# Performance work log

Hardware: AMD Instinct MI355X
Metric: run time of the kernel (lower is better)

The kernel has to match this reference:

```python
import jax, jax.numpy as jnp
import numpy as np

N, S, F, E, H, O, L, FE = 8, 1024, 64, 512, 8, 64, 6, 4
HD = E // H
FF = FE * E


def setup_inputs() -> dict:
    key = jax.random.key(0)
    ks = iter(jax.random.split(key, 40))
    def rn(shape, s=0.02):
        return jax.random.normal(next(ks), shape, jnp.float32) * s
    return {
        'x': jax.random.normal(next(ks), (N, F, S), jnp.float32),
        'W_first': rn((F, E)), 'b_first': jnp.zeros((E,), jnp.float32),
        'pos_emb': rn((S, E)),
        'Wq': rn((L, HD, HD)), 'bq': jnp.zeros((L, HD), jnp.float32),
        'Wk': rn((L, HD, HD)), 'bk': jnp.zeros((L, HD), jnp.float32),
        'Wv': rn((L, HD, HD)), 'bv': jnp.zeros((L, HD), jnp.float32),
        'Wo': rn((L, E, E)), 'bo': jnp.zeros((L, E), jnp.float32),
        'g1': jnp.ones((L, E), jnp.float32), 'be1': jnp.zeros((L, E), jnp.float32),
        'Wf1': rn((L, E, FF)), 'bf1': jnp.zeros((L, FF), jnp.float32),
        'Wf2': rn((L, FF, E)), 'bf2': jnp.zeros((L, E), jnp.float32),
        'g2': jnp.ones((L, E), jnp.float32), 'be2': jnp.zeros((L, E), jnp.float32),
        'Wfin': rn((E, O)), 'bfin': jnp.zeros((O,), jnp.float32),
    }


def layernorm(x, g, b, eps=1e-5):
    m = jnp.mean(x, axis=-1, keepdims=True)
    v = jnp.mean(jnp.square(x - m), axis=-1, keepdims=True)
    return (x - m) * jax.lax.rsqrt(v + eps) * g + b


def reference(x, W_first, b_first, pos_emb, Wq, bq, Wk, bk, Wv, bv, Wo, bo,
              g1, be1, Wf1, bf1, Wf2, bf2, g2, be2, Wfin, bfin):
    # x: (N, F, S) -> (N, S, F)
    h = jax.nn.relu(jnp.einsum('nfs,fe->nse', x, W_first) + b_first) + pos_emb[None]
    scale = E ** 0.5  # note: module scales by sqrt(embed_size), not sqrt(head_dim)
    for i in range(L):
        t = h.reshape(N, S, H, HD)
        q = jnp.einsum('nshd,de->nshe', t, Wq[i]) + bq[i]
        k = jnp.einsum('nshd,de->nshe', t, Wk[i]) + bk[i]
        v = jnp.einsum('nshd,de->nshe', t, Wv[i]) + bv[i]
        energy = jnp.einsum('nqhd,nkhd->nhqk', q, k)  # (N,H,S,S)
        att = jax.nn.softmax(energy / scale, axis=-1)
        o = jnp.einsum('nhqk,nkhd->nqhd', att, v).reshape(N, S, E)
        o = jnp.einsum('nse,ef->nsf', o, Wo[i]) + bo[i]
        hx = layernorm(o + h, g1[i], be1[i])
        ff = jax.nn.relu(jnp.einsum('nse,ef->nsf', hx, Wf1[i]) + bf1[i])
        ff = jnp.einsum('nsf,fe->nse', ff, Wf2[i]) + bf2[i]
        h = layernorm(ff + hx, g2[i], be2[i])
    # Conv1d kernel_size=1 == pointwise linear over channels; output (N, O, S)
    return jnp.einsum('nse,eo->nos', h, Wfin) + bfin[None, :, None]
```

## Files before the change

kernel.cpp:

```cpp
#include <hip/hip_runtime.h>
#include <hip/hip_bf16.h>
#include <math.h>

#define N_ 8
#define S_ 1024
#define F_ 64
#define E_ 512
#define H_ 8
#define O_ 64
#define L_ 6
#define HD_ 64
#define FF_ 2048
#define SCALE_ 0.044194173824159216f
#define LOG2E_ 1.4426950408889634f
#define QSCALE_ (SCALE_ * LOG2E_)

typedef unsigned short u16;
typedef __attribute__((ext_vector_type(8))) unsigned short u16x8;
typedef __attribute__((ext_vector_type(8))) short short8;
typedef __attribute__((ext_vector_type(4))) float floatx4;

__device__ __forceinline__ u16 f2b(float f) {
    union { float f; unsigned u; } v; v.f = f;
    unsigned u = v.u;
    unsigned r = (u + 0x7FFFu + ((u >> 16) & 1u)) >> 16;
    return (u16)r;
}
__device__ __forceinline__ u16 f2b_fast(float f) {
    union { float f; unsigned u; } v; v.f = f;
    return (u16)((v.u + 0x8000u) >> 16);
}
__device__ __forceinline__ int pperm(int row) {
    return ((2 * (row >> 2) + 5 * (row & 3)) & 7) | ((row & 2) << 2);
}

__global__ __launch_bounds__(256) void first_mfma(
    const float* __restrict__ x, const u16* __restrict__ wt,
    const float* __restrict__ bf, const float* __restrict__ pe,
    float* __restrict__ hout, u16* __restrict__ hb)
{
    __shared__ u16 a_s[128][72];
    int t = threadIdx.x;
    int w = t >> 6, lane = t & 63, quad = lane >> 4, c16 = lane & 15;
    int rowhalf = w >> 1, colhalf = w & 1;
    int col0 = blockIdx.x * 128;
    int row0 = blockIdx.y * 128;
    int n = row0 >> 10, s0 = row0 & 1023;

    const float* xb = x + (size_t)n * F_ * S_ + s0;
    #pragma unroll
    for (int i = 0; i < 8; i++) {
        int pos = (t + i * 256) * 4;
        int f = pos >> 7, sl = pos & 127;
        float4 v = *(const float4*)&xb[(size_t)f * S_ + sl];
        a_s[sl + 0][f] = f2b_fast(v.x);
        a_s[sl + 1][f] = f2b_fast(v.y);
        a_s[sl + 2][f] = f2b_fast(v.z);
        a_s[sl + 3][f] = f2b_fast(v.w);
    }
    __syncthreads();

    floatx4 acc[4][4];
    #pragma unroll
    for (int mt = 0; mt < 4; mt++)
        #pragma unroll
        for (int nt = 0; nt < 4; nt++) acc[mt][nt] = (floatx4){0.f, 0.f, 0.f, 0.f};

    #pragma unroll
    for (int ks = 0; ks < 2; ks++) {
        short8 af[4], bfr[4];
        #pragma unroll
        for (int mt = 0; mt < 4; mt++)
            af[mt] = *(const short8*)&a_s[rowhalf * 64 + mt * 16 + c16][ks * 32 + quad * 8];
        #pragma unroll
        for (int nt = 0; nt < 4; nt++)
            bfr[nt] = *(const short8*)&wt[(size_t)(col0 + colhalf * 64 + nt * 16 + c16) * F_
                                          + ks * 32 + quad * 8];
        #pragma unroll
        for (int mt = 0; mt < 4; mt++)
            #pragma unroll
            for (int nt = 0; nt < 4; nt++)
                acc[mt][nt] = __builtin_amdgcn_mfma_f32_16x16x32_bf16(
                    af[mt], bfr[nt], acc[mt][nt], 0, 0, 0);
    }

    #pragma unroll
    for (int nt = 0; nt < 4; nt++) {
        int col = col0 + colhalf * 64 + nt * 16 + c16;
        float bv = bf[col];
        #pragma unroll
        for (int mt = 0; mt < 4; mt++) {
            #pragma unroll
            for (int r = 0; r < 4; r++) {
                size_t row = (size_t)row0 + rowhalf * 64 + mt * 16 + quad * 4 + r;
                int s = (int)(row & 1023);
                float v = fmaxf(acc[mt][nt][r] + bv, 0.f) + pe[(size_t)s * E_ + col];
                hout[row * E_ + col] = v;
                hb[row * E_ + col] = f2b_fast(v);
            }
        }
    }
}

__global__ __launch_bounds__(256) void wcast_t(
    const float* __restrict__ W0, u16* __restrict__ Wt0, int K, int Nc)
{
    __shared__ float tile[32][33];
    int t = threadIdx.x;
    int bx = blockIdx.x, by = blockIdx.y;
    const float* W = W0 + (size_t)blockIdx.z * K * Nc;
    u16* Wt = Wt0 + (size_t)blockIdx.z * K * Nc;
    #pragma unroll
    for (int i = 0; i < 4; i++) {
        int q = t + i * 256; int r = q >> 5, c = q & 31;
        tile[r][c] = W[(size_t)(by * 32 + r) * Nc + bx * 32 + c];
    }
    __syncthreads();
    #pragma unroll
    for (int i = 0; i < 4; i++) {
        int q = t + i * 256; int r = q >> 5, c = q & 31;
        Wt[(size_t)(bx * 32 + r) * K + by * 32 + c] = f2b(tile[c][r]);
    }
}

__global__ __launch_bounds__(256) void qkvw_cast(
    const float* __restrict__ Wq, const float* __restrict__ Wk,
    const float* __restrict__ Wv,
    u16* __restrict__ wqt, u16* __restrict__ wkt, u16* __restrict__ wvt)
{
    int l = blockIdx.x;
    int t = threadIdx.x;
    size_t off = (size_t)l * HD_ * HD_;
    #pragma unroll
    for (int i = 0; i < 16; i++) {
        int idx = t + i * 256;
        int e = idx >> 6, d = idx & 63;
        wqt[off + idx] = f2b(Wq[off + d * HD_ + e]);
        wkt[off + idx] = f2b(Wk[off + d * HD_ + e]);
        wvt[off + idx] = f2b(Wv[off + d * HD_ + e]);
    }
}

__global__ __launch_bounds__(256) void qkv_mfma(
    const u16* __restrict__ hb,
    const u16* __restrict__ wqt, const u16* __restrict__ wkt,
    const u16* __restrict__ wvt,
    const float* __restrict__ bq, const float* __restrict__ bk,
    const float* __restrict__ bv,
    u16* __restrict__ qo, u16* __restrict__ ko, u16* __restrict__ vo)
{
    __shared__ u16 a_s[256][72];
    int t = threadIdx.x;
    int w = t >> 6, lane = t & 63, quad = lane >> 4, c16 = lane & 15;
    size_t row0 = (size_t)blockIdx.x * 256;

    #pragma unroll
    for (int i = 0; i < 8; i++) {
        int q = t + i * 256; int r = q >> 3, c = q & 7;
        *(u16x8*)&a_s[r][c * 8] = *(const u16x8*)&hb[(row0 + r) * HD_ + c * 8];
    }
    __syncthreads();

    short8 af[4][2];
    #pragma unroll
    for (int mt = 0; mt < 4; mt++)
        #pragma unroll
        for (int ks = 0; ks < 2; ks++)
            af[mt][ks] = *(const short8*)&a_s[w * 64 + mt * 16 + c16][ks * 32 + quad * 8];

    const u16* wts[3] = {wqt, wkt, wvt};
    const float* bs[3] = {bq, bk, bv};
    u16* outs[3] = {qo, ko, vo};

    #pragma unroll
    for (int m = 0; m < 3; m++) {
        short8 bfr[4][2];
        #pragma unroll
        for (int nt = 0; nt < 4; nt++)
            #pragma unroll
            for (int ks = 0; ks < 2; ks++)
                bfr[nt][ks] = *(const short8*)&wts[m][(nt * 16 + c16) * HD_ + ks * 32 + quad * 8];
        floatx4 acc[4][4];
        #pragma unroll
        for (int mt = 0; mt < 4; mt++)
            #pragma unroll
            for (int nt = 0; nt < 4; nt++) acc[mt][nt] = (floatx4){0.f, 0.f, 0.f, 0.f};
        #pragma unroll
        for (int ks = 0; ks < 2; ks++)
            #pragma unroll
            for (int mt = 0; mt < 4; mt++)
                #pragma unroll
                for (int nt = 0; nt < 4; nt++)
                    acc[mt][nt] = __builtin_amdgcn_mfma_f32_16x16x32_bf16(
                        af[mt][ks], bfr[nt][ks], acc[mt][nt], 0, 0, 0);
        float osc = (m == 0) ? QSCALE_ : 1.0f;
        #pragma unroll
        for (int nt = 0; nt < 4; nt++) {
            float bv_ = bs[m][nt * 16 + c16];
            #pragma unroll
            for (int mt = 0; mt < 4; mt++)
                #pragma unroll
                for (int r = 0; r < 4; r++)
                    outs[m][(row0 + w * 64 + mt * 16 + quad * 4 + r) * HD_ + nt * 16 + c16] =
                        f2b_fast((acc[mt][nt][r] + bv_) * osc);
        }
    }
}

__global__ __launch_bounds__(256) void vtrans(
    const u16* __restrict__ vb, u16* __restrict__ vt)
{
    int bid = blockIdx.x;
    int st = bid & 15, hh = (bid >> 4) & 7, n = bid >> 7;
    __shared__ u16 tile[64][72];
    int t = threadIdx.x;
    #pragma unroll
    for (int i = 0; i < 2; i++) {
        int q = t + i * 256; int sl = q >> 3, c = q & 7;
        *(u16x8*)&tile[sl][c * 8] =
            *(const u16x8*)&vb[(((size_t)(n * S_ + st * 64 + sl)) * H_ + hh) * 64 + c * 8];
    }
    __syncthreads();
    #pragma unroll
    for (int i = 0; i < 2; i++) {
        int q = t + i * 256; int d = q >> 3, sc = q & 7;
        u16x8 v;
        #pragma unroll
        for (int j = 0; j < 8; j++) v[j] = tile[sc * 8 + j][d];
        *(u16x8*)&vt[((size_t)(n * H_ + hh) * 64 + d) * (size_t)S_ + st * 64 + sc * 8] = v;
    }
}

__global__ __launch_bounds__(256, 2) void attn_mfma(
    const u16* __restrict__ Q, const u16* __restrict__ K,
    const u16* __restrict__ Vt, u16* __restrict__ O)
{
    int bid = blockIdx.x;
    int qt = bid & 7, hh = (bid >> 3) & 7, n = bid >> 6;
    int t = threadIdx.x;
    int w = t >> 6, lane = t & 63, quad = lane >> 4, c16 = lane & 15;

    __shared__ u16 q_s[128][72];
    __shared__ u16 k_s[64][72];
    __shared__ u16 vt_s[64][72];
    __shared__ u16 p_s[4][32][72];

    const size_t qkbase = (size_t)n * S_ * E_ + hh * 64;
    const size_t vtbase = ((size_t)(n * H_ + hh) * 64) * (size_t)S_;

    #pragma unroll
    for (int i = 0; i < 4; i++) {
        int q = t + i * 256; int r = q >> 3, c = q & 7;
        *(u16x8*)&q_s[r][c * 8] =
            *(const u16x8*)&Q[qkbase + (size_t)(qt * 128 + r) * E_ + c * 8];
    }
    __syncthreads();

    short8 af[2][2];
    #pragma unroll
    for (int mt = 0; mt < 2; mt++)
        #pragma unroll
        for (int ks = 0; ks < 2; ks++)
            af[mt][ks] = *(const short8*)&q_s[w * 32 + mt * 16 + c16][ks * 32 + quad * 8];

    const short8 ones = {(short)0x3F80, (short)0x3F80, (short)0x3F80, (short)0x3F80,
                         (short)0x3F80, (short)0x3F80, (short)0x3F80, (short)0x3F80};
    const int pr = pperm(c16);
    int pw[4];
    #pragma unroll
    for (int r = 0; r < 4; r++) pw[r] = pperm(quad * 4 + r);

    floatx4 oacc[2][4], lacc[2];
    #pragma unroll
    for (int mt = 0; mt < 2; mt++) {
        lacc[mt] = (floatx4){0.f, 0.f, 0.f, 0.f};
        #pragma unroll
        for (int nt = 0; nt < 4; nt++) oacc[mt][nt] = (floatx4){0.f, 0.f, 0.f, 0.f};
    }

    for (int k0 = 0; k0 < S_; k0 += 64) {
        #pragma unroll
        for (int i = 0; i < 2; i++) {
            int q = t + i * 256; int r = q >> 3, c = q & 7;
            *(u16x8*)&k_s[r][c * 8] =
                *(const u16x8*)&K[qkbase + (size_t)(k0 + r) * E_ + c * 8];
            *(u16x8*)&vt_s[r][c * 8] =
                *(const u16x8*)&Vt[vtbase + (size_t)r * S_ + k0 + c * 8];
        }
        __syncthreads();

        floatx4 sc[2][4];
        #pragma unroll
        for (int mt = 0; mt < 2; mt++)
            #pragma unroll
            for (int nt = 0; nt < 4; nt++) sc[mt][nt] = (floatx4){0.f, 0.f, 0.f, 0.f};
        #pragma unroll
        for (int ks = 0; ks < 2; ks++) {
            short8 bfr[4];
            #pragma unroll
            for (int nt = 0; nt < 4; nt++)
                bfr[nt] = *(const short8*)&k_s[nt * 16 + c16][ks * 32 + quad * 8];
            #pragma unroll
            for (int mt = 0; mt < 2; mt++)
                #pragma unroll
                for (int nt = 0; nt < 4; nt++)
                    sc[mt][nt] = __builtin_amdgcn_mfma_f32_16x16x32_bf16(
                        af[mt][ks], bfr[nt], sc[mt][nt], 0, 0, 0);
        }

        #pragma unroll
        for (int mt = 0; mt < 2; mt++)
            #pragma unroll
            for (int nt = 0; nt < 4; nt++)
                #pragma unroll
                for (int r = 0; r < 4; r++)
                    p_s[w][mt * 16 + pw[r]][nt * 16 + c16] =
                        f2b_fast(exp2f(sc[mt][nt][r]));

        #pragma unroll
        for (int ks = 0; ks < 2; ks++) {
            short8 vf[4];
            #pragma unroll
            for (int nt = 0; nt < 4; nt++)
                vf[nt] = *(const short8*)&vt_s[nt * 16 + c16][ks * 32 + quad * 8];
            #pragma unroll
            for (int mt = 0; mt < 2; mt++) {
                short8 pf = *(const short8*)&p_s[w][mt * 16 + pr][ks * 32 + quad * 8];
                lacc[mt] = __builtin_amdgcn_mfma_f32_16x16x32_bf16(pf, ones, lacc[mt], 0, 0, 0);
                #pragma unroll
                for (int nt = 0; nt < 4; nt++)
                    oacc[mt][nt] = __builtin_amdgcn_mfma_f32_16x16x32_bf16(
                        pf, vf[nt], oacc[mt][nt], 0, 0, 0);
            }
        }
        __syncthreads();
    }

    #pragma unroll
    for (int mt = 0; mt < 2; mt++)
        #pragma unroll
        for (int r = 0; r < 4; r++) {
            float rl = 1.f / lacc[mt][r];
            int s = qt * 128 + w * 32 + mt * 16 + quad * 4 + r;
            size_t base = (size_t)(n * S_ + s) * E_ + hh * 64;
            #pragma unroll
            for (int nt = 0; nt < 4; nt++)
                O[base + nt * 16 + c16] = f2b_fast(oacc[mt][nt][r] * rl);
        }
}

template <bool RELU, bool HASRES, bool OUTF32, bool OUTBF16>
__global__ __launch_bounds__(256) void gemm_mfma(
    const u16* __restrict__ A, const u16* __restrict__ Bt,
    const float* __restrict__ bias, const float* __restrict__ resid,
    float* __restrict__ outf, u16* __restrict__ outb, int M, int Nc, int K)
{
    __shared__ u16 a_s[128][72];
    __shared__ u16 b_s[128][72];
    int t = threadIdx.x;
    int w = t >> 6, lane = t & 63, quad = lane >> 4, c16 = lane & 15;
    int rowhalf = w >> 1, colhalf = w & 1;
    size_t row0 = (size_t)blockIdx.y * 128;
    size_t col0 = (size_t)blockIdx.x * 128;

    floatx4 acc[4][4];
    #pragma unroll
    for (int mt = 0; mt < 4; mt++)
        #pragma unroll
        for (int nt = 0; nt < 4; nt++) acc[mt][nt] = (floatx4){0.f, 0.f, 0.f, 0.f};

    for (int k0 = 0; k0 < K; k0 += 64) {
        #pragma unroll
        for (int i = 0; i < 4; i++) {
            int q = t + i * 256; int r = q >> 3, c = q & 7;
            *(u16x8*)&a_s[r][c * 8] = *(const u16x8*)&A[(row0 + r) * K + k0 + c * 8];
            *(u16x8*)&b_s[r][c * 8] = *(const u16x8*)&Bt[(col0 + r) * K + k0 + c * 8];
        }
        __syncthreads();
        #pragma unroll
        for (int ks = 0; ks < 2; ks++) {
            short8 af[4], bf[4];
            #pragma unroll
            for (int mt = 0; mt < 4; mt++)
                af[mt] = *(const short8*)&a_s[rowhalf * 64 + mt * 16 + c16][ks * 32 + quad * 8];
            #pragma unroll
            for (int nt = 0; nt < 4; nt++)
                bf[nt] = *(const short8*)&b_s[colhalf * 64 + nt * 16 + c16][ks * 32 + quad * 8];
            #pragma unroll
            for (int mt = 0; mt < 4; mt++)
                #pragma unroll
                for (int nt = 0; nt < 4; nt++)
                    acc[mt][nt] = __builtin_amdgcn_mfma_f32_16x16x32_bf16(
                        af[mt], bf[nt], acc[mt][nt], 0, 0, 0);
        }
        __syncthreads();
    }

    #pragma unroll
    for (int nt = 0; nt < 4; nt++) {
        int col = (int)col0 + colhalf * 64 + nt * 16 + c16;
        float bv = bias[col];
        #pragma unroll
        for (int mt = 0; mt < 4; mt++) {
            size_t rowb = row0 + rowhalf * 64 + mt * 16 + quad * 4;
            #pragma unroll
            for (int r = 0; r < 4; r++) {
                size_t row = rowb + r;
                float v = acc[mt][nt][r] + bv;
                if constexpr (HASRES) v += resid[row * Nc + col];
                if constexpr (RELU) v = fmaxf(v, 0.f);
                if constexpr (OUTF32) outf[row * Nc + col] = v;
                if constexpr (OUTBF16) outb[row * Nc + col] = f2b_fast(v);
            }
        }
    }
}

template <bool EMITB>
__global__ __launch_bounds__(256) void layernorm_k(
    const float* __restrict__ in, const float* __restrict__ g,
    const float* __restrict__ bb, float* __restrict__ out, u16* __restrict__ outb)
{
    int row = blockIdx.x;
    int t = threadIdx.x;
    const float* x = in + (size_t)row * E_;
    float x0 = x[t], x1 = x[t + 256];
    float s = x0 + x1;
    #pragma unroll
    for (int off = 32; off; off >>= 1) s += __shfl_down(s, off, 64);
    __shared__ float red[4];
    int wid = t >> 6, lane = t & 63;
    if (lane == 0) red[wid] = s;
    __syncthreads();
    float m = (red[0] + red[1] + red[2] + red[3]) * (1.f / E_);
    float d0 = x0 - m, d1 = x1 - m;
    float sq = d0 * d0 + d1 * d1;
    #pragma unroll
    for (int off = 32; off; off >>= 1) sq += __shfl_down(sq, off, 64);
    __syncthreads();
    if (lane == 0) red[wid] = sq;
    __syncthreads();
    float var = (red[0] + red[1] + red[2] + red[3]) * (1.f / E_);
    float rstd = rsqrtf(var + 1e-5f);
    float o0 = d0 * rstd * g[t] + bb[t];
    float o1 = d1 * rstd * g[t + 256] + bb[t + 256];
    out[(size_t)row * E_ + t] = o0;
    out[(size_t)row * E_ + t + 256] = o1;
    if constexpr (EMITB) {
        outb[(size_t)row * E_ + t] = f2b_fast(o0);
        outb[(size_t)row * E_ + t + 256] = f2b_fast(o1);
    }
}

__global__ __launch_bounds__(256) void final_mfma(
    const u16* __restrict__ hb, const u16* __restrict__ wft,
    const float* __restrict__ bfin, float* __restrict__ outp)
{
    __shared__ u16 a_s[64][72];
    int t = threadIdx.x;
    int w = t >> 6, lane = t & 63, quad = lane >> 4, c16 = lane & 15;
    size_t row0 = (size_t)blockIdx.x * 64;

    floatx4 acc[4];
    #pragma unroll
    for (int nt = 0; nt < 4; nt++) acc[nt] = (floatx4){0.f, 0.f, 0.f, 0.f};

    for (int k0 = 0; k0 < E_; k0 += 64) {
        #pragma unroll
        for (int i = 0; i < 2; i++) {
            int q = t + i * 256; int r = q >> 3, c = q & 7;
            *(u16x8*)&a_s[r][c * 8] = *(const u16x8*)&hb[(row0 + r) * E_ + k0 + c * 8];
        }
        __syncthreads();
        #pragma unroll
        for (int ks = 0; ks < 2; ks++) {
            short8 af = *(const short8*)&a_s[w * 16 + c16][ks * 32 + quad * 8];
            #pragma unroll
            for (int nt = 0; nt < 4; nt++) {
                short8 bf = *(const short8*)&wft[(nt * 16 + c16) * E_ + k0 + ks * 32 + quad * 8];
                acc[nt] = __builtin_amdgcn_mfma_f32_16x16x32_bf16(af, bf, acc[nt], 0, 0, 0);
            }
        }
        __syncthreads();
    }

    #pragma unroll
    for (int nt = 0; nt < 4; nt++) {
        int o = nt * 16 + c16;
        float bv = bfin[o];
        #pragma unroll
        for (int r = 0; r < 4; r++) {
            size_t row = row0 + w * 16 + quad * 4 + r;
            int n = (int)(row >> 10), s = (int)(row & 1023);
            outp[((size_t)(n * O_ + o)) * S_ + s] = acc[nt][r] + bv;
        }
    }
}

extern "C" void kernel_launch(void* const* d_in, const int* in_sizes, int n_in,
                              void* d_out, int out_size, void* d_ws, size_t ws_size,
                              hipStream_t stream)
{
    const float* x       = (const float*)d_in[0];
    const float* W_first = (const float*)d_in[1];
    const float* b_first = (const float*)d_in[2];
    const float* pos_emb = (const float*)d_in[3];
    const float* Wq      = (const float*)d_in[4];
    const float* bq      = (const float*)d_in[5];
    const float* Wk      = (const float*)d_in[6];
    const float* bk      = (const float*)d_in[7];
    const float* Wv      = (const float*)d_in[8];
    const float* bv      = (const float*)d_in[9];
    const float* Wo      = (const float*)d_in[10];
    const float* bo      = (const float*)d_in[11];
    const float* g1      = (const float*)d_in[12];
    const float* be1     = (const float*)d_in[13];
    const float* Wf1     = (const float*)d_in[14];
    const float* bf1     = (const float*)d_in[15];
    const float* Wf2     = (const float*)d_in[16];
    const float* bf2     = (const float*)d_in[17];
    const float* g2      = (const float*)d_in[18];
    const float* be2     = (const float*)d_in[19];
    const float* Wfin    = (const float*)d_in[20];
    const float* bfin    = (const float*)d_in[21];
    float* out = (float*)d_out;

    const size_t M4 = (size_t)N_ * S_ * E_;
    float* hbuf = (float*)d_ws;
    float* t1   = hbuf + M4;
    float* hx   = t1 + M4;
    u16*   hxb  = (u16*)(hx + M4);
    u16*   hb   = hxb;
    u16*   qb   = hxb + M4;
    u16*   kb   = qb + M4;
    u16*   vb   = kb + M4;
    u16*   vt   = vb + M4;
    u16*   ob   = vt + M4;
    u16*   ffb  = qb;
    u16*   wot  = ob + M4;
    u16*   wf1t = wot + (size_t)L_ * E_ * E_;
    u16*   wf2t = wf1t + (size_t)L_ * E_ * FF_;
    u16*   wqt  = wf2t + (size_t)L_ * FF_ * E_;
    u16*   wkt  = wqt + (size_t)L_ * HD_ * HD_;
    u16*   wvt  = wkt + (size_t)L_ * HD_ * HD_;
    u16*   wft  = wvt + (size_t)L_ * HD_ * HD_;
    u16*   w1t  = wft + (size_t)O_ * E_;

    const int rows = N_ * S_;

    qkvw_cast<<<L_, 256, 0, stream>>>(Wq, Wk, Wv, wqt, wkt, wvt);
    wcast_t<<<dim3(E_ / 32, F_ / 32, 1), 256, 0, stream>>>(W_first, w1t, F_, E_);
    wcast_t<<<dim3(E_ / 32, E_ / 32, L_), 256, 0, stream>>>(Wo, wot, E_, E_);
    wcast_t<<<dim3(FF_ / 32, E_ / 32, L_), 256, 0, stream>>>(Wf1, wf1t, E_, FF_);
    wcast_t<<<dim3(E_ / 32, FF_ / 32, L_), 256, 0, stream>>>(Wf2, wf2t, FF_, E_);
    wcast_t<<<dim3(O_ / 32, E_ / 32, 1), 256, 0, stream>>>(Wfin, wft, E_, O_);

    first_mfma<<<dim3(E_ / 128, rows / 128), 256, 0, stream>>>(
        x, w1t, b_first, pos_emb, hbuf, hb);

    for (int i = 0; i < L_; i++) {
        qkv_mfma<<<256, 256, 0, stream>>>(
            hb, wqt + (size_t)i * HD_ * HD_, wkt + (size_t)i * HD_ * HD_,
            wvt + (size_t)i * HD_ * HD_, bq + i * HD_, bk + i * HD_, bv + i * HD_,
            qb, kb, vb);
        vtrans<<<1024, 256, 0, stream>>>(vb, vt);
        attn_mfma<<<512, 256, 0, stream>>>(qb, kb, vt, ob);
        gemm_mfma<false, true, true, false><<<dim3(E_ / 128, rows / 128), 256, 0, stream>>>(
            ob, wot + (size_t)i * E_ * E_, bo + i * E_, hbuf, t1, nullptr, rows, E_, E_);
        layernorm_k<true><<<rows, 256, 0, stream>>>(t1, g1 + i * E_, be1 + i * E_, hx, hxb);
        gemm_mfma<true, false, false, true><<<dim3(FF_ / 128, rows / 128), 256, 0, stream>>>(
            hxb, wf1t + (size_t)i * E_ * FF_, bf1 + i * FF_, nullptr, nullptr, ffb,
            rows, FF_, E_);
        gemm_mfma<false, true, true, false><<<dim3(E_ / 128, rows / 128), 256, 0, stream>>>(
            ffb, wf2t + (size_t)i * FF_ * E_, bf2 + i * E_, hx, t1, nullptr,
            rows, E_, FF_);
        layernorm_k<true><<<rows, 256, 0, stream>>>(t1, g2 + i * E_, be2 + i * E_, hbuf, hb);
    }

    final_mfma<<<rows / 64, 256, 0, stream>>>(hb, wft, bfin, out);
}
```

Before: 1.157 ms.

## Register-prefetch next K tiles in GEMM/attention loops and halve M tile for E-wide GEMMs

```diff
diff --git a/kernel.cpp b/kernel.cpp
--- a/kernel.cpp
+++ b/kernel.cpp
@@ -278,14 +278,26 @@
         for (int nt = 0; nt < 4; nt++) oacc[mt][nt] = (floatx4){0.f, 0.f, 0.f, 0.f};
     }
 
+    int ar = t >> 3, acq = (t & 7) * 8;
+    u16x8 pk[2], pv[2];
+    #pragma unroll
+    for (int i = 0; i < 2; i++) {
+        pk[i] = *(const u16x8*)&K[qkbase + (size_t)(ar + i * 32) * E_ + acq];
+        pv[i] = *(const u16x8*)&Vt[vtbase + (size_t)(ar + i * 32) * S_ + acq];
+    }
+
     for (int k0 = 0; k0 < S_; k0 += 64) {
         #pragma unroll
         for (int i = 0; i < 2; i++) {
-            int q = t + i * 256; int r = q >> 3, c = q & 7;
-            *(u16x8*)&k_s[r][c * 8] =
-                *(const u16x8*)&K[qkbase + (size_t)(k0 + r) * E_ + c * 8];
-            *(u16x8*)&vt_s[r][c * 8] =
-                *(const u16x8*)&Vt[vtbase + (size_t)r * S_ + k0 + c * 8];
+            *(u16x8*)&k_s[ar + i * 32][acq] = pk[i];
+            *(u16x8*)&vt_s[ar + i * 32][acq] = pv[i];
+        }
+        if (k0 + 64 < S_) {
+            #pragma unroll
+            for (int i = 0; i < 2; i++) {
+                pk[i] = *(const u16x8*)&K[qkbase + (size_t)(k0 + 64 + ar + i * 32) * E_ + acq];
+                pv[i] = *(const u16x8*)&Vt[vtbase + (size_t)(ar + i * 32) * S_ + k0 + 64 + acq];
+            }
         }
         __syncthreads();
 
@@ -349,45 +361,63 @@
         }
 }
 
-template <bool RELU, bool HASRES, bool OUTF32, bool OUTBF16>
+template <int MT, bool RELU, bool HASRES, bool OUTF32, bool OUTBF16>
 __global__ __launch_bounds__(256) void gemm_mfma(
     const u16* __restrict__ A, const u16* __restrict__ Bt,
     const float* __restrict__ bias, const float* __restrict__ resid,
     float* __restrict__ outf, u16* __restrict__ outb, int M, int Nc, int K)
 {
-    __shared__ u16 a_s[128][72];
+    constexpr int MTILES = MT / 32;
+    __shared__ u16 a_s[MT][72];
     __shared__ u16 b_s[128][72];
     int t = threadIdx.x;
     int w = t >> 6, lane = t & 63, quad = lane >> 4, c16 = lane & 15;
     int rowhalf = w >> 1, colhalf = w & 1;
-    size_t row0 = (size_t)blockIdx.y * 128;
+    size_t row0 = (size_t)blockIdx.y * MT;
     size_t col0 = (size_t)blockIdx.x * 128;
 
-    floatx4 acc[4][4];
-    #pragma unroll
-    for (int mt = 0; mt < 4; mt++)
+    floatx4 acc[MTILES][4];
+    #pragma unroll
+    for (int mt = 0; mt < MTILES; mt++)
         #pragma unroll
         for (int nt = 0; nt < 4; nt++) acc[mt][nt] = (floatx4){0.f, 0.f, 0.f, 0.f};
 
+    int ar = t >> 3, acq = (t & 7) * 8;
+    u16x8 pa[MTILES], pb[4];
+    #pragma unroll
+    for (int i = 0; i < MTILES; i++)
+        pa[i] = *(const u16x8*)&A[(row0 + ar + i * 32) * K + acq];
+    #pragma unroll
+    for (int i = 0; i < 4; i++)
+        pb[i] = *(const u16x8*)&Bt[(col0 + ar + i * 32) * K + acq];
+
     for (int k0 = 0; k0 < K; k0 += 64) {
         #pragma unroll
-        for (int i = 0; i < 4; i++) {
-            int q = t + i * 256; int r = q >> 3, c = q & 7;
-            *(u16x8*)&a_s[r][c * 8] = *(const u16x8*)&A[(row0 + r) * K + k0 + c * 8];
-            *(u16x8*)&b_s[r][c * 8] = *(const u16x8*)&Bt[(col0 + r) * K + k0 + c * 8];
+        for (int i = 0; i < MTILES; i++)
+            *(u16x8*)&a_s[ar + i * 32][acq] = pa[i];
+        #pragma unroll
+        for (int i = 0; i < 4; i++)
+            *(u16x8*)&b_s[ar + i * 32][acq] = pb[i];
+        if (k0 + 64 < K) {
+            #pragma unroll
+            for (int i = 0; i < MTILES; i++)
+                pa[i] = *(const u16x8*)&A[(row0 + ar + i * 32) * K + k0 + 64 + acq];
+            #pragma unroll
+            for (int i = 0; i < 4; i++)
+                pb[i] = *(const u16x8*)&Bt[(col0 + ar + i * 32) * K + k0 + 64 + acq];
         }
         __syncthreads();
         #pragma unroll
         for (int ks = 0; ks < 2; ks++) {
-            short8 af[4], bf[4];
-            #pragma unroll
-            for (int mt = 0; mt < 4; mt++)
-                af[mt] = *(const short8*)&a_s[rowhalf * 64 + mt * 16 + c16][ks * 32 + quad * 8];
+            short8 af[MTILES], bf[4];
+            #pragma unroll
+            for (int mt = 0; mt < MTILES; mt++)
+                af[mt] = *(const short8*)&a_s[rowhalf * (MT / 2) + mt * 16 + c16][ks * 32 + quad * 8];
             #pragma unroll
             for (int nt = 0; nt < 4; nt++)
                 bf[nt] = *(const short8*)&b_s[colhalf * 64 + nt * 16 + c16][ks * 32 + quad * 8];
             #pragma unroll
-            for (int mt = 0; mt < 4; mt++)
+            for (int mt = 0; mt < MTILES; mt++)
                 #pragma unroll
                 for (int nt = 0; nt < 4; nt++)
                     acc[mt][nt] = __builtin_amdgcn_mfma_f32_16x16x32_bf16(
@@ -401,8 +431,8 @@
         int col = (int)col0 + colhalf * 64 + nt * 16 + c16;
         float bv = bias[col];
         #pragma unroll
-        for (int mt = 0; mt < 4; mt++) {
-            size_t rowb = row0 + rowhalf * 64 + mt * 16 + quad * 4;
+        for (int mt = 0; mt < MTILES; mt++) {
+            size_t rowb = row0 + rowhalf * (MT / 2) + mt * 16 + quad * 4;
             #pragma unroll
             for (int r = 0; r < 4; r++) {
                 size_t row = rowb + r;
@@ -465,11 +495,20 @@
     #pragma unroll
     for (int nt = 0; nt < 4; nt++) acc[nt] = (floatx4){0.f, 0.f, 0.f, 0.f};
 
+    int ar = t >> 3, acq = (t & 7) * 8;
+    u16x8 pa[2];
+    #pragma unroll
+    for (int i = 0; i < 2; i++)
+        pa[i] = *(const u16x8*)&hb[(row0 + ar + i * 32) * E_ + acq];
+
     for (int k0 = 0; k0 < E_; k0 += 64) {
         #pragma unroll
-        for (int i = 0; i < 2; i++) {
-            int q = t + i * 256; int r = q >> 3, c = q & 7;
-            *(u16x8*)&a_s[r][c * 8] = *(const u16x8*)&hb[(row0 + r) * E_ + k0 + c * 8];
+        for (int i = 0; i < 2; i++)
+            *(u16x8*)&a_s[ar + i * 32][acq] = pa[i];
+        if (k0 + 64 < E_) {
+            #pragma unroll
+            for (int i = 0; i < 2; i++)
+                pa[i] = *(const u16x8*)&hb[(row0 + ar + i * 32) * E_ + k0 + 64 + acq];
         }
         __syncthreads();
         #pragma unroll
@@ -565,13 +604,13 @@
             qb, kb, vb);
         vtrans<<<1024, 256, 0, stream>>>(vb, vt);
         attn_mfma<<<512, 256, 0, stream>>>(qb, kb, vt, ob);
-        gemm_mfma<false, true, true, false><<<dim3(E_ / 128, rows / 128), 256, 0, stream>>>(
+        gemm_mfma<64, false, true, true, false><<<dim3(E_ / 128, rows / 64), 256, 0, stream>>>(
             ob, wot + (size_t)i * E_ * E_, bo + i * E_, hbuf, t1, nullptr, rows, E_, E_);
         layernorm_k<true><<<rows, 256, 0, stream>>>(t1, g1 + i * E_, be1 + i * E_, hx, hxb);
-        gemm_mfma<true, false, false, true><<<dim3(FF_ / 128, rows / 128), 256, 0, stream>>>(
+        gemm_mfma<128, true, false, false, true><<<dim3(FF_ / 128, rows / 128), 256, 0, stream>>>(
             hxb, wf1t + (size_t)i * E_ * FF_, bf1 + i * FF_, nullptr, nullptr, ffb,
             rows, FF_, E_);
-        gemm_mfma<false, true, true, false><<<dim3(E_ / 128, rows / 128), 256, 0, stream>>>(
+        gemm_mfma<64, false, true, true, false><<<dim3(E_ / 128, rows / 64), 256, 0, stream>>>(
             ffb, wf2t + (size_t)i * FF_ * E_, bf2 + i * E_, hx, t1, nullptr,
             rows, E_, FF_);
         layernorm_k<true><<<rows, 256, 0, stream>>>(t1, g2 + i * E_, be2 + i * E_, hbuf, hb);
```

Result: faster. 1.056 ms (-8.7%).
